# Kernel tuning notes

Hardware: AMD Instinct MI355X
Metric: run time of the kernel (lower is better)

The kernel has to match this reference:

```python
import jax, jax.numpy as jnp
import numpy as np

B, T, D = 4, 2048, 1024

def layer_norm(x, gamma, bias):
    # NOTE: faithfully reproduces the source's (buggy) LN: x - mu/sqrt(var), unbiased var
    mu = jnp.mean(x, axis=-1, keepdims=True)
    var = jnp.var(x, axis=-1, ddof=1, keepdims=True)
    return (x - mu / jnp.sqrt(var)) * gamma + bias

def setup_inputs() -> dict:
    key = jax.random.key(0)
    ks = jax.random.split(key, 8)
    scale = 1.0 / np.sqrt(D)
    return {
        'x': jax.random.normal(ks[0], (B, T, D), dtype=jnp.float32),
        'gamma1': jnp.ones((D,), jnp.float32),
        'beta1': jnp.zeros((D,), jnp.float32),
        'w_q': jax.random.uniform(ks[1], (D, D), jnp.float32, -scale, scale),
        'w_k': jax.random.uniform(ks[2], (D, D), jnp.float32, -scale, scale),
        'w_v': jax.random.uniform(ks[3], (D, D), jnp.float32, -scale, scale),
        'gamma2': jnp.ones((D,), jnp.float32),
        'beta2': jnp.zeros((D,), jnp.float32),
        'W1': jax.random.uniform(ks[4], (D, D), jnp.float32, -scale, scale),
        'b1': jnp.zeros((D,), jnp.float32),
        'W2': jax.random.uniform(ks[5], (D, D), jnp.float32, -scale, scale),
        'b2': jnp.zeros((D,), jnp.float32),
    }

def reference(x, gamma1, beta1, w_q, w_k, w_v, gamma2, beta2, W1, b1, W2, b2):
    d_model = x.shape[-1]
    t = x.shape[1]
    h = layer_norm(x, gamma1, beta1)
    q = jnp.einsum('btk,kd->btd', h, w_q)
    k = jnp.einsum('btk,kd->btd', h, w_k)
    v = jnp.einsum('btk,kd->btd', h, w_v)
    scale = 1.0 / jnp.sqrt(jnp.asarray(d_model, x.dtype))
    causal = jnp.tril(jnp.ones((t, t), dtype=bool))
    mask = jnp.where(causal, 0.0, -jnp.inf).astype(x.dtype)
    scores = jnp.einsum('bqd,bkd->bqk', q, k) * scale + mask
    attn = jax.nn.softmax(scores, axis=-1)
    y = jnp.einsum('bqt,btd->bqd', attn, v) + x
    h2 = layer_norm(y, gamma2, beta2)
    out = jnp.maximum(h2 @ W1 + b1, 0.0) @ W2 + b2
    return out + y
```

## Files before the change

### kernel.cpp

```cpp
#include <hip/hip_runtime.h>
#include <hip/hip_bf16.h>
#include <math.h>

using bf16 = __hip_bfloat16;

static constexpr int Bn = 4;
static constexpr int Tn = 2048;
static constexpr int Dn = 1024;

typedef __attribute__((ext_vector_type(8))) short bf16x8;
typedef __attribute__((ext_vector_type(4))) float f32x4;

__device__ __forceinline__ float ldf(float v) { return v; }
__device__ __forceinline__ float ldf(bf16 v) { return __bfloat162float(v); }
__device__ __forceinline__ bf16 f2b(float v) { return __float2bfloat16(v); }
__device__ __forceinline__ float b2f(short s) {
    return __uint_as_float(((unsigned)(unsigned short)s) << 16);
}
__device__ __forceinline__ short f2bs(float v) {
    bf16 t = __float2bfloat16(v);
    return *reinterpret_cast<short*>(&t);
}

template <typename T> __device__ __forceinline__ T from_float(float v);
template <> __device__ __forceinline__ float from_float<float>(float v) { return v; }
template <> __device__ __forceinline__ bf16 from_float<bf16>(float v) { return f2b(v); }

__device__ __forceinline__ void load4(const float* p, float* v) {
    const float4 t = *(const float4*)p;
    v[0] = t.x; v[1] = t.y; v[2] = t.z; v[3] = t.w;
}
__device__ __forceinline__ void load4(const bf16* p, float* v) {
    const short4 t = *(const short4*)p;
    v[0] = b2f(t.x); v[1] = b2f(t.y); v[2] = b2f(t.z); v[3] = b2f(t.w);
}

__device__ __forceinline__ void async_copy16(const bf16* g, bf16* l) {
    __builtin_amdgcn_global_load_lds(
        (const __attribute__((address_space(1))) void*)g,
        (__attribute__((address_space(3))) void*)l,
        16, 0, 0);
}

template <int BN, int EPI, typename OutT, bool RELU>
__global__ __launch_bounds__(512, 2) void gemm8p(
    const bf16* __restrict__ A, const bf16* __restrict__ Bm,
    OutT* __restrict__ C, const float* __restrict__ bias,
    const bf16* __restrict__ res, bf16* __restrict__ vtp,
    int K, int lda, int ldb, int ldc)
{
    static_assert(EPI != 1 || BN == 128, "V-transpose epilogue needs BN=128");
    constexpr int BM = 256, BK = 32;
    constexpr int NT = BN / 64;
    constexpr int BUFE = (BM + BN) * BK;
    __shared__ __align__(16) bf16 smem[3 * BUFE];

    const int bm = blockIdx.x, bn = blockIdx.y;
    const int tid = threadIdx.x;
    const int wave = tid >> 6;
    const int lane = tid & 63;
    const int wm = wave >> 2;
    const int wn = wave & 3;
    const int lr = lane >> 2;
    const int lc = (lane & 3) * 8;
    const int arow = lane & 15;
    const int kq = (lane >> 4) * 8;

    const int NK = K / BK;

    const bf16* gA0 = A + (size_t)(bm * BM + wave * 16 + lr) * lda + lc;
    const bf16* gA1 = A + (size_t)(bm * BM + (wave + 8) * 16 + lr) * lda + lc;
    const bf16* gB0 = Bm + (size_t)(bn * BN + wave * 16 + lr) * ldb + lc;
    const bf16* gB1 = (BN == 256)
        ? Bm + (size_t)(bn * BN + (wave + 8) * 16 + lr) * ldb + lc : nullptr;

    f32x4 acc[8][NT] = {};

    {
        bf16* As0 = smem;
        bf16* Bs0 = smem + BM * BK;
        bf16* As1 = smem + BUFE;
        bf16* Bs1 = smem + BUFE + BM * BK;
        async_copy16(gA0, As0 + wave * 512);
        async_copy16(gA1, As0 + (wave + 8) * 512);
        async_copy16(gB0, Bs0 + wave * 512);
        if constexpr (BN == 256) async_copy16(gB1, Bs0 + (wave + 8) * 512);
        async_copy16(gA0 + BK, As1 + wave * 512);
        async_copy16(gA1 + BK, As1 + (wave + 8) * 512);
        async_copy16(gB0 + BK, Bs1 + wave * 512);
        if constexpr (BN == 256) async_copy16(gB1 + BK, Bs1 + (wave + 8) * 512);
    }
    if constexpr (BN == 256) asm volatile("s_waitcnt vmcnt(4)" ::: "memory");
    else                     asm volatile("s_waitcnt vmcnt(3)" ::: "memory");
    __builtin_amdgcn_s_barrier();

    int cb = 0;
    int sb = 2;
    for (int kt = 0; kt < NK; ++kt) {
        const bf16* As = smem + cb * BUFE;
        const bf16* Bs = As + BM * BK;
        const bool st = (kt + 2) < NK;
        const int koff = (kt + 2) * BK;

        bf16x8 af[8], bf0[NT / 2];
#pragma unroll
        for (int mt = 0; mt < 8; ++mt)
            af[mt] = *(const bf16x8*)&As[(wm * 8 + mt) * 512 + arow * 32 + kq];
#pragma unroll
        for (int nt = 0; nt < NT / 2; ++nt)
            bf0[nt] = *(const bf16x8*)&Bs[(wn * NT + nt) * 512 + arow * 32 + kq];
        if (st) {
            bf16* Ad = smem + sb * BUFE;
            async_copy16(gA0 + koff, Ad + wave * 512);
            async_copy16(gA1 + koff, Ad + (wave + 8) * 512);
        }
        __builtin_amdgcn_s_barrier();
        asm volatile("s_waitcnt lgkmcnt(0)" ::: "memory");
        __builtin_amdgcn_sched_barrier(0);
        __builtin_amdgcn_s_setprio(1);
#pragma unroll
        for (int mt = 0; mt < 8; ++mt)
#pragma unroll
            for (int nt = 0; nt < NT / 2; ++nt)
                acc[mt][nt] = __builtin_amdgcn_mfma_f32_16x16x32_bf16(
                    af[mt], bf0[nt], acc[mt][nt], 0, 0, 0);
        __builtin_amdgcn_s_setprio(0);
        __builtin_amdgcn_s_barrier();

        bf16x8 bf1[NT / 2];
#pragma unroll
        for (int nt = 0; nt < NT / 2; ++nt)
            bf1[nt] = *(const bf16x8*)&Bs[(wn * NT + NT / 2 + nt) * 512 + arow * 32 + kq];
        if (st) {
            bf16* Bd = smem + sb * BUFE + BM * BK;
            async_copy16(gB0 + koff, Bd + wave * 512);
            if constexpr (BN == 256) async_copy16(gB1 + koff, Bd + (wave + 8) * 512);
        }
        __builtin_amdgcn_s_barrier();
        asm volatile("s_waitcnt lgkmcnt(0)" ::: "memory");
        __builtin_amdgcn_sched_barrier(0);
        __builtin_amdgcn_s_setprio(1);
#pragma unroll
        for (int mt = 0; mt < 8; ++mt)
#pragma unroll
            for (int nt = 0; nt < NT / 2; ++nt)
                acc[mt][NT / 2 + nt] = __builtin_amdgcn_mfma_f32_16x16x32_bf16(
                    af[mt], bf1[nt], acc[mt][NT / 2 + nt], 0, 0, 0);
        __builtin_amdgcn_s_setprio(0);
        if (st) {
            if constexpr (BN == 256) asm volatile("s_waitcnt vmcnt(4)" ::: "memory");
            else                     asm volatile("s_waitcnt vmcnt(3)" ::: "memory");
        } else {
            asm volatile("s_waitcnt vmcnt(0)" ::: "memory");
        }
        __builtin_amdgcn_s_barrier();

        cb = (cb + 1 == 3) ? 0 : cb + 1;
        sb = (sb + 1 == 3) ? 0 : sb + 1;
    }

    const int qrow = (lane >> 4) * 4;
    const int ccol = lane & 15;

    if constexpr (EPI == 1) {
        bf16* tt = smem;
#pragma unroll
        for (int mt = 0; mt < 8; ++mt)
#pragma unroll
            for (int nt = 0; nt < NT; ++nt) {
                const int dl = wn * (NT * 16) + nt * 16 + ccol;
                const int tl = wm * 128 + mt * 16 + qrow;
                short4 o;
                o.x = f2bs(acc[mt][nt][0]);
                o.y = f2bs(acc[mt][nt][1]);
                o.z = f2bs(acc[mt][nt][2]);
                o.w = f2bs(acc[mt][nt][3]);
                *(short4*)&tt[dl * 264 + tl] = o;
            }
        __syncthreads();
        const int b = (bm * BM) >> 11;
        const int tin = (bm * BM) & (Tn - 1);
        const int dr = tid >> 4;
        const int t0 = (tid & 15) * 16;
#pragma unroll
        for (int p = 0; p < 4; ++p) {
            const int d = p * 32 + dr;
            const bf16* srcl = &tt[d * 264 + t0];
            bf16* dst = vtp + ((size_t)b * Dn + bn * BN + d) * Tn + tin + t0;
            ((bf16x8*)dst)[0] = ((const bf16x8*)srcl)[0];
            ((bf16x8*)dst)[1] = ((const bf16x8*)srcl)[1];
        }
        return;
    }

    const int row0 = bm * BM + wm * 128;
    const int col0 = bn * BN + wn * (NT * 16);
#pragma unroll
    for (int mt = 0; mt < 8; ++mt)
#pragma unroll
        for (int nt = 0; nt < NT; ++nt) {
            const int cc = col0 + nt * 16 + ccol;
            const float bv = bias ? bias[cc] : 0.0f;
#pragma unroll
            for (int r = 0; r < 4; ++r) {
                const int rr = row0 + mt * 16 + qrow + r;
                float v = acc[mt][nt][r] + bv;
                if (RELU) v = fmaxf(v, 0.0f);
                if (res) v += b2f(*(const short*)&res[(size_t)rr * ldc + cc]);
                C[(size_t)rr * ldc + cc] = from_float<OutT>(v);
            }
        }
}

template <int BM, int BN, int MINW, int EPI, typename OutT, typename ResT, bool RELU>
__global__ __launch_bounds__(256, MINW) void gemm_nt(
    const bf16* __restrict__ A, const bf16* __restrict__ Bm,
    OutT* __restrict__ C, const float* __restrict__ bias,
    const ResT* __restrict__ res, float* __restrict__ rowsum,
    int M, int N, int K, int lda, int ldb, int ldc,
    long sA, long sB, long sC, long sR, int mode)
{
    int bm, bn, bz;
    if (mode >= 3) {
        bn = blockIdx.x; bz = blockIdx.y;
        bm = (int)gridDim.z - 1 - (int)blockIdx.z;
    } else {
        bm = blockIdx.x; bn = blockIdx.y; bz = blockIdx.z;
    }
    if (mode == 4 && bn * BN > bm * BM + (BM - 1)) return;
    const int kend = bm * BM + BM;
    const int kmax = (mode == 3) ? (kend < K ? kend : K) : K;

    const bf16* Ab = A + (size_t)bz * sA;
    const bf16* Bb = Bm + (size_t)bz * sB;

    constexpr int WROWS = BM / 64;
    constexpr int WCOLS = 4 / WROWS;
    constexpr int TM = 64;
    constexpr int TN = BN / WCOLS;
    constexpr int MT = TM / 16;
    constexpr int NT = TN / 16;
    constexpr int nA = BM / 16;
    constexpr int nB = BN / 16;
    constexpr int STAGE = 2 * (BM + BN) * 32;

    __shared__ __align__(16) bf16 smem[STAGE];
    bf16* As = smem;
    bf16* Bs = smem + 2 * BM * 32;

    const int tid = threadIdx.x;
    const int wave = tid >> 6;
    const int lane = tid & 63;
    const int wm = wave / WCOLS;
    const int wn = wave % WCOLS;

    f32x4 acc[MT][NT] = {};

    const int lr = lane >> 2;
    const int lc = (lane & 3) * 8;
    const bf16* gAc[nA / 4]; bf16* lAc[nA / 4];
    const bf16* gBc[nB / 4]; bf16* lBc[nB / 4];
#pragma unroll
    for (int i = 0; i < nA / 4; ++i) {
        const int c = wave + 4 * i;
        gAc[i] = Ab + (size_t)(bm * BM + c * 16 + lr) * lda + lc;
        lAc[i] = &As[c * 512];
    }
#pragma unroll
    for (int i = 0; i < nB / 4; ++i) {
        const int c = wave + 4 * i;
        gBc[i] = Bb + (size_t)(bn * BN + c * 16 + lr) * ldb + lc;
        lBc[i] = &Bs[c * 512];
    }

    const int arow = lane & 15;
    const int kq = (lane >> 4) * 8;

    for (int k0 = 0; k0 < kmax; k0 += 64) {
#pragma unroll
        for (int hh = 0; hh < 2; ++hh) {
#pragma unroll
            for (int i = 0; i < nA / 4; ++i)
                async_copy16(gAc[i] + k0 + 32 * hh, lAc[i] + hh * (BM * 32));
#pragma unroll
            for (int i = 0; i < nB / 4; ++i)
                async_copy16(gBc[i] + k0 + 32 * hh, lBc[i] + hh * (BN * 32));
        }
        __syncthreads();

#pragma unroll
        for (int hh = 0; hh < 2; ++hh) {
            const bf16* Ah = As + hh * (BM * 32);
            const bf16* Bh = Bs + hh * (BN * 32);
            bf16x8 af[MT], bfm[NT];
#pragma unroll
            for (int t = 0; t < MT; ++t)
                af[t] = *(const bf16x8*)&Ah[(wm * TM + t * 16 + arow) * 32 + kq];
#pragma unroll
            for (int t = 0; t < NT; ++t)
                bfm[t] = *(const bf16x8*)&Bh[(wn * TN + t * 16 + arow) * 32 + kq];
#pragma unroll
            for (int mt = 0; mt < MT; ++mt)
#pragma unroll
                for (int nt = 0; nt < NT; ++nt)
                    acc[mt][nt] = __builtin_amdgcn_mfma_f32_16x16x32_bf16(
                        af[mt], bfm[nt], acc[mt][nt], 0, 0, 0);
        }
        __syncthreads();
    }

    const int rowBase = bm * BM + wm * TM;
    const int colBase = bn * BN + wn * TN;
    const int qrow = (lane >> 4) * 4;
    const int ccol = lane & 15;

    if (EPI == 2) {
        OutT* Cb = C + (size_t)bz * sC;
        float* rsb = rowsum + (size_t)bz * Tn;
        const float scale = 0.03125f;
#pragma unroll
        for (int mt = 0; mt < MT; ++mt) {
            float rsv[4] = {0.f, 0.f, 0.f, 0.f};
#pragma unroll
            for (int nt = 0; nt < NT; ++nt) {
                const int cc = colBase + nt * 16 + ccol;
#pragma unroll
                for (int r = 0; r < 4; ++r) {
                    const int rr = rowBase + mt * 16 + qrow + r;
                    float e = 0.0f;
                    if (cc <= rr) {
                        const short es = f2bs(__expf(acc[mt][nt][r] * scale));
                        Cb[(size_t)rr * ldc + cc] = *(const bf16*)&es;
                        e = b2f(es);
                    } else {
                        Cb[(size_t)rr * ldc + cc] = from_float<OutT>(0.0f);
                    }
                    rsv[r] += e;
                }
            }
#pragma unroll
            for (int r = 0; r < 4; ++r) {
                float v = rsv[r];
                v += __shfl_xor(v, 1);
                v += __shfl_xor(v, 2);
                v += __shfl_xor(v, 4);
                v += __shfl_xor(v, 8);
                if (ccol == 0)
                    atomicAdd(rsb + rowBase + mt * 16 + qrow + r, v);
            }
        }
        return;
    }

    OutT* Cb = C + (size_t)bz * sC;
    const ResT* Rb = res ? (res + (size_t)bz * sR) : nullptr;
    const float* rsb = (EPI == 3) ? (rowsum + (size_t)bz * Tn) : nullptr;
#pragma unroll
    for (int mt = 0; mt < MT; ++mt) {
        float inv4[4];
        if (EPI == 3) {
#pragma unroll
            for (int r = 0; r < 4; ++r)
                inv4[r] = 1.0f / rsb[rowBase + mt * 16 + qrow + r];
        }
#pragma unroll
        for (int nt = 0; nt < NT; ++nt) {
            const int cc = colBase + nt * 16 + ccol;
            const float bv = bias ? bias[cc] : 0.0f;
#pragma unroll
            for (int r = 0; r < 4; ++r) {
                const int rr = rowBase + mt * 16 + qrow + r;
                float v = acc[mt][nt][r];
                if (EPI == 3) v *= inv4[r];
                v += bv;
                if (RELU) v = fmaxf(v, 0.0f);
                if (Rb) v += ldf(Rb[(size_t)rr * ldc + cc]);
                Cb[(size_t)rr * ldc + cc] = from_float<OutT>(v);
            }
        }
    }
}

template <typename InT>
__device__ __forceinline__ void ln_row(
    const InT* __restrict__ xr, const float* __restrict__ gamma,
    const float* __restrict__ beta, bf16* __restrict__ orow, int tid)
{
    const int j = tid * 4;
    float v[4];
    load4(xr + j, v);
    float s = v[0] + v[1] + v[2] + v[3];
    float sq = v[0] * v[0] + v[1] * v[1] + v[2] * v[2] + v[3] * v[3];
#pragma unroll
    for (int o = 32; o > 0; o >>= 1) {
        s += __shfl_down(s, o);
        sq += __shfl_down(sq, o);
    }
    __shared__ float red[2][4];
    const int lane = tid & 63, w = tid >> 6;
    if (lane == 0) { red[0][w] = s; red[1][w] = sq; }
    __syncthreads();
    s  = red[0][0] + red[0][1] + red[0][2] + red[0][3];
    sq = red[1][0] + red[1][1] + red[1][2] + red[1][3];
    const float mean = s / (float)Dn;
    const float var = (sq - s * s / (float)Dn) / (float)(Dn - 1);
    const float coef = mean * rsqrtf(var);

    const float4 g = *(const float4*)(gamma + j);
    const float4 be = *(const float4*)(beta + j);
    short4 o;
    o.x = f2bs((v[0] - coef) * g.x + be.x);
    o.y = f2bs((v[1] - coef) * g.y + be.y);
    o.z = f2bs((v[2] - coef) * g.z + be.z);
    o.w = f2bs((v[3] - coef) * g.w + be.w);
    *(short4*)(orow + j) = o;
}

template <typename InT>
__global__ __launch_bounds__(256) void ln_kernel(
    const InT* __restrict__ x, const float* __restrict__ gamma,
    const float* __restrict__ beta, bf16* __restrict__ out)
{
    const int row = blockIdx.x;
    ln_row(x + (size_t)row * Dn, gamma, beta, out + (size_t)row * Dn, threadIdx.x);
}

struct WPtrs { const float* p[5]; };

__global__ __launch_bounds__(256) void prep_kernel(
    WPtrs wp, bf16* __restrict__ wdst, float* __restrict__ rowsum,
    const float* __restrict__ x, const float* __restrict__ gamma1,
    const float* __restrict__ beta1, bf16* __restrict__ h)
{
    const int bx = blockIdx.x;
    if (bx < 5120) {
        __shared__ bf16 tile[32][33];
        const int z = bx >> 10;
        const int t = bx & 1023;
        const float* src = wp.p[z];
        bf16* d = wdst + (size_t)z * Dn * Dn;
        const int c0 = (t & 31) * 32, r0 = (t >> 5) * 32;
        const int tx = threadIdx.x & 31;
        const int ty = threadIdx.x >> 5;
#pragma unroll
        for (int dy = 0; dy < 32; dy += 8)
            tile[ty + dy][tx] = f2b(src[(size_t)(r0 + ty + dy) * Dn + (c0 + tx)]);
        __syncthreads();
#pragma unroll
        for (int dy = 0; dy < 32; dy += 8)
            d[(size_t)(c0 + ty + dy) * Dn + (r0 + tx)] = tile[tx][ty + dy];
    } else if (bx < 5128) {
        const int base = (bx - 5120) * 1024;
#pragma unroll
        for (int i = 0; i < 4; ++i) rowsum[base + i * 256 + threadIdx.x] = 0.0f;
    } else {
        const int row = bx - 5128;
        ln_row(x + (size_t)row * Dn, gamma1, beta1, h + (size_t)row * Dn, threadIdx.x);
    }
}

extern "C" void kernel_launch(void* const* d_in, const int* in_sizes, int n_in,
                              void* d_out, int out_size, void* d_ws, size_t ws_size,
                              hipStream_t stream) {
    const float* x      = (const float*)d_in[0];
    const float* gamma1 = (const float*)d_in[1];
    const float* beta1  = (const float*)d_in[2];
    const float* w_q    = (const float*)d_in[3];
    const float* w_k    = (const float*)d_in[4];
    const float* w_v    = (const float*)d_in[5];
    const float* gamma2 = (const float*)d_in[6];
    const float* beta2  = (const float*)d_in[7];
    const float* W1     = (const float*)d_in[8];
    const float* b1     = (const float*)d_in[9];
    const float* W2     = (const float*)d_in[10];
    const float* b2     = (const float*)d_in[11];
    float* out = (float*)d_out;

    char* ws = (char*)d_ws;
    size_t off = 0;
    auto alloc = [&](size_t bytes) {
        char* p = ws + off;
        off += (bytes + 255) & ~(size_t)255;
        return p;
    };
    const size_t BT = (size_t)Bn * Tn;
    bf16* h    = (bf16*)alloc(BT * Dn * 2);
    bf16* qk   = (bf16*)alloc(BT * 2 * Dn * 2);
    bf16* vt   = (bf16*)alloc(BT * Dn * 2);
    bf16* wbuf = (bf16*)alloc((size_t)5 * Dn * Dn * 2);
    bf16* S    = (bf16*)alloc((size_t)Bn * Tn * Tn * 2);
    bf16* y    = (bf16*)alloc(BT * Dn * 2);
    float* rowsum = (float*)alloc((size_t)Bn * Tn * 4);
    bf16* h2   = h;
    bf16* mid  = qk;

    const dim3 blk(256);
    const dim3 blk512(512);
    const long TD  = (long)Tn * Dn;
    const long TT  = (long)Tn * Tn;
    const long TD2 = (long)Tn * 2 * Dn;
    const size_t DD = (size_t)Dn * Dn;

    WPtrs wp; wp.p[0] = w_q; wp.p[1] = w_k; wp.p[2] = w_v; wp.p[3] = W1; wp.p[4] = W2;
    prep_kernel<<<dim3(5128 + (unsigned)BT, 1, 1), blk, 0, stream>>>(
        wp, wbuf, rowsum, x, gamma1, beta1, h);

    gemm8p<256, 0, bf16, false><<<dim3(32, 8, 1), blk512, 0, stream>>>(
        h, wbuf, qk, nullptr, nullptr, nullptr, Dn, Dn, Dn, 2 * Dn);

    gemm8p<128, 1, bf16, false><<<dim3(32, 8, 1), blk512, 0, stream>>>(
        h, wbuf + 2 * DD, (bf16*)nullptr, nullptr, nullptr, vt,
        Dn, Dn, Dn, 0);

    gemm_nt<128, 128, 4, 2, bf16, float, false><<<dim3(16, Bn, 16), blk, 0, stream>>>(
        qk, qk + 1024, S, nullptr, nullptr, rowsum,
        Tn, Tn, Dn, 2 * Dn, 2 * Dn, Tn, TD2, TD2, TT, 0, 4);

    gemm_nt<128, 128, 4, 3, bf16, float, false><<<dim3(8, Bn, 16), blk, 0, stream>>>(
        S, vt, y, nullptr, x, rowsum,
        Tn, Dn, Tn, Tn, Tn, Dn, TT, TD, TD, TD, 3);

    ln_kernel<bf16><<<dim3((unsigned)BT), blk, 0, stream>>>(y, gamma2, beta2, h2);

    gemm_nt<128, 128, 4, 0, bf16, float, true><<<dim3(64, 8, 1), blk, 0, stream>>>(
        h2, wbuf + 3 * DD, mid, b1, nullptr, nullptr,
        (int)BT, Dn, Dn, Dn, Dn, Dn, 0, 0, 0, 0, 0);

    gemm_nt<128, 128, 4, 0, float, bf16, false><<<dim3(64, 8, 1), blk, 0, stream>>>(
        mid, wbuf + 4 * DD, out, b2, y, nullptr,
        (int)BT, Dn, Dn, Dn, Dn, Dn, 0, 0, 0, 0, 0);
}
```

Before: 351.4 us.

## Split causal PV GEMM along K into two halves and fuse reduction into LN2

The attention P·V GEMM's causal K range is split into two chunks per row-block. Each chunk writes an fp32 partial result to its own buffer, which doubles the grid and balances the triangular workload. The new ln2_fused kernel sums the two partials, applies the softmax row normalisation and the residual x, writes y, and computes the second layernorm in one pass. This adds fp32 partial-buffer traffic (a new workspace buffer plus reuse of qk) in exchange for more parallelism and one less separate normalisation pass.

```diff
diff --git a/kernel.cpp b/kernel.cpp
--- a/kernel.cpp
+++ b/kernel.cpp
@@ -215,21 +215,33 @@
 template <int BM, int BN, int MINW, int EPI, typename OutT, typename ResT, bool RELU>
 __global__ __launch_bounds__(256, MINW) void gemm_nt(
     const bf16* __restrict__ A, const bf16* __restrict__ Bm,
-    OutT* __restrict__ C, const float* __restrict__ bias,
+    OutT* __restrict__ C, float* __restrict__ c2,
+    const float* __restrict__ bias,
     const ResT* __restrict__ res, float* __restrict__ rowsum,
     int M, int N, int K, int lda, int ldb, int ldc,
     long sA, long sB, long sC, long sR, int mode)
 {
-    int bm, bn, bz;
-    if (mode >= 3) {
+    int bm, bn, bz, chunk = 0;
+    if (mode == 5) {
+        bn = blockIdx.x; bz = blockIdx.y;
+        const int zc = blockIdx.z;
+        bm = 15 - (zc >> 1);
+        chunk = zc & 1;
+    } else if (mode == 4) {
         bn = blockIdx.x; bz = blockIdx.y;
         bm = (int)gridDim.z - 1 - (int)blockIdx.z;
     } else {
         bm = blockIdx.x; bn = blockIdx.y; bz = blockIdx.z;
     }
     if (mode == 4 && bn * BN > bm * BM + (BM - 1)) return;
-    const int kend = bm * BM + BM;
-    const int kmax = (mode == 3) ? (kend < K ? kend : K) : K;
+
+    int kbeg = 0, kmax = K;
+    if (mode == 5) {
+        const int keff = (bm + 1) * BM;
+        const int half = keff >> 1;
+        kbeg = chunk ? half : 0;
+        kmax = chunk ? keff : half;
+    }
 
     const bf16* Ab = A + (size_t)bz * sA;
     const bf16* Bb = Bm + (size_t)bz * sB;
@@ -276,7 +288,7 @@
     const int arow = lane & 15;
     const int kq = (lane >> 4) * 8;
 
-    for (int k0 = 0; k0 < kmax; k0 += 64) {
+    for (int k0 = kbeg; k0 < kmax; k0 += 64) {
 #pragma unroll
         for (int hh = 0; hh < 2; ++hh) {
 #pragma unroll
@@ -353,16 +365,10 @@
     }
 
     OutT* Cb = C + (size_t)bz * sC;
+    if (mode == 5 && chunk) Cb = (OutT*)(c2 + (size_t)bz * sC);
     const ResT* Rb = res ? (res + (size_t)bz * sR) : nullptr;
-    const float* rsb = (EPI == 3) ? (rowsum + (size_t)bz * Tn) : nullptr;
 #pragma unroll
     for (int mt = 0; mt < MT; ++mt) {
-        float inv4[4];
-        if (EPI == 3) {
-#pragma unroll
-            for (int r = 0; r < 4; ++r)
-                inv4[r] = 1.0f / rsb[rowBase + mt * 16 + qrow + r];
-        }
 #pragma unroll
         for (int nt = 0; nt < NT; ++nt) {
             const int cc = colBase + nt * 16 + ccol;
@@ -370,9 +376,7 @@
 #pragma unroll
             for (int r = 0; r < 4; ++r) {
                 const int rr = rowBase + mt * 16 + qrow + r;
-                float v = acc[mt][nt][r];
-                if (EPI == 3) v *= inv4[r];
-                v += bv;
+                float v = acc[mt][nt][r] + bv;
                 if (RELU) v = fmaxf(v, 0.0f);
                 if (Rb) v += ldf(Rb[(size_t)rr * ldc + cc]);
                 Cb[(size_t)rr * ldc + cc] = from_float<OutT>(v);
@@ -416,13 +420,55 @@
     *(short4*)(orow + j) = o;
 }
 
-template <typename InT>
-__global__ __launch_bounds__(256) void ln_kernel(
-    const InT* __restrict__ x, const float* __restrict__ gamma,
-    const float* __restrict__ beta, bf16* __restrict__ out)
+__global__ __launch_bounds__(256) void ln2_fused(
+    const float* __restrict__ yp0, const float* __restrict__ yp1,
+    const float* __restrict__ rowsum, const float* __restrict__ x,
+    const float* __restrict__ gamma, const float* __restrict__ beta,
+    bf16* __restrict__ y, bf16* __restrict__ h2)
 {
     const int row = blockIdx.x;
-    ln_row(x + (size_t)row * Dn, gamma, beta, out + (size_t)row * Dn, threadIdx.x);
+    const int tid = threadIdx.x;
+    const int j = tid * 4;
+    const size_t base = (size_t)row * Dn;
+    const float inv = 1.0f / rowsum[row];
+
+    float p0[4], p1[4], xv[4], v[4];
+    load4(yp0 + base + j, p0);
+    load4(yp1 + base + j, p1);
+    load4(x + base + j, xv);
+    short4 yo;
+    v[0] = (p0[0] + p1[0]) * inv + xv[0];
+    v[1] = (p0[1] + p1[1]) * inv + xv[1];
+    v[2] = (p0[2] + p1[2]) * inv + xv[2];
+    v[3] = (p0[3] + p1[3]) * inv + xv[3];
+    yo.x = f2bs(v[0]); yo.y = f2bs(v[1]); yo.z = f2bs(v[2]); yo.w = f2bs(v[3]);
+    *(short4*)(y + base + j) = yo;
+
+    float s = v[0] + v[1] + v[2] + v[3];
+    float sq = v[0] * v[0] + v[1] * v[1] + v[2] * v[2] + v[3] * v[3];
+#pragma unroll
+    for (int o = 32; o > 0; o >>= 1) {
+        s += __shfl_down(s, o);
+        sq += __shfl_down(sq, o);
+    }
+    __shared__ float red[2][4];
+    const int lane = tid & 63, w = tid >> 6;
+    if (lane == 0) { red[0][w] = s; red[1][w] = sq; }
+    __syncthreads();
+    s  = red[0][0] + red[0][1] + red[0][2] + red[0][3];
+    sq = red[1][0] + red[1][1] + red[1][2] + red[1][3];
+    const float mean = s / (float)Dn;
+    const float var = (sq - s * s / (float)Dn) / (float)(Dn - 1);
+    const float coef = mean * rsqrtf(var);
+
+    const float4 g = *(const float4*)(gamma + j);
+    const float4 be = *(const float4*)(beta + j);
+    short4 o;
+    o.x = f2bs((v[0] - coef) * g.x + be.x);
+    o.y = f2bs((v[1] - coef) * g.y + be.y);
+    o.z = f2bs((v[2] - coef) * g.z + be.z);
+    o.w = f2bs((v[3] - coef) * g.w + be.w);
+    *(short4*)(h2 + base + j) = o;
 }
 
 struct WPtrs { const float* p[5]; };
@@ -491,6 +537,8 @@
     bf16* S    = (bf16*)alloc((size_t)Bn * Tn * Tn * 2);
     bf16* y    = (bf16*)alloc(BT * Dn * 2);
     float* rowsum = (float*)alloc((size_t)Bn * Tn * 4);
+    float* yp1 = (float*)alloc(BT * Dn * 4);
+    float* yp0 = (float*)qk;
     bf16* h2   = h;
     bf16* mid  = qk;
 
@@ -513,20 +561,21 @@
         Dn, Dn, Dn, 0);
 
     gemm_nt<128, 128, 4, 2, bf16, float, false><<<dim3(16, Bn, 16), blk, 0, stream>>>(
-        qk, qk + 1024, S, nullptr, nullptr, rowsum,
+        qk, qk + 1024, S, nullptr, nullptr, nullptr, rowsum,
         Tn, Tn, Dn, 2 * Dn, 2 * Dn, Tn, TD2, TD2, TT, 0, 4);
 
-    gemm_nt<128, 128, 4, 3, bf16, float, false><<<dim3(8, Bn, 16), blk, 0, stream>>>(
-        S, vt, y, nullptr, x, rowsum,
-        Tn, Dn, Tn, Tn, Tn, Dn, TT, TD, TD, TD, 3);
-
-    ln_kernel<bf16><<<dim3((unsigned)BT), blk, 0, stream>>>(y, gamma2, beta2, h2);
+    gemm_nt<128, 128, 4, 0, float, float, false><<<dim3(8, Bn, 32), blk, 0, stream>>>(
+        S, vt, yp0, yp1, nullptr, nullptr, nullptr,
+        Tn, Dn, Tn, Tn, Tn, Dn, TT, TD, TD, 0, 5);
+
+    ln2_fused<<<dim3((unsigned)BT), blk, 0, stream>>>(
+        yp0, yp1, rowsum, x, gamma2, beta2, y, h2);
 
     gemm_nt<128, 128, 4, 0, bf16, float, true><<<dim3(64, 8, 1), blk, 0, stream>>>(
-        h2, wbuf + 3 * DD, mid, b1, nullptr, nullptr,
+        h2, wbuf + 3 * DD, mid, nullptr, b1, nullptr, nullptr,
         (int)BT, Dn, Dn, Dn, Dn, Dn, 0, 0, 0, 0, 0);
 
     gemm_nt<128, 128, 4, 0, float, bf16, false><<<dim3(64, 8, 1), blk, 0, stream>>>(
-        mid, wbuf + 4 * DD, out, b2, y, nullptr,
+        mid, wbuf + 4 * DD, out, nullptr, b2, y, nullptr,
         (int)BT, Dn, Dn, Dn, Dn, Dn, 0, 0, 0, 0, 0);
 }
```

After: 352.4 us. Within noise of the previous version (+0.3%).
